# Optimization experiments

Measured on AMD Instinct MI355X. Metric: run time of the kernel, lower is better.

Reference implementation:

```python
import jax, jax.numpy as jnp
import numpy as np

B, N, DM = 8, 1024, 512
H, D = 8, 64  # heads, dim_head; inner_dim = H*D = 512

def setup_inputs() -> dict:
    key = jax.random.key(0)
    k1, k2, k3, k4, k5 = jax.random.split(key, 5)
    s = 1.0 / np.sqrt(DM)
    return {
        "current": jax.random.normal(k1, (B, N, DM), dtype=jnp.float32),
        "hidden": jax.random.normal(k2, (B, N, DM), dtype=jnp.float32),
        "Wq": jax.random.normal(k3, (DM, H * D), dtype=jnp.float32) * s,
        "Wkv": jax.random.normal(k4, (DM, 2 * H * D), dtype=jnp.float32) * s,
        "Wo": jax.random.normal(k5, (H * D, H * D), dtype=jnp.float32) * s,
    }

def reference(current, hidden, Wq, Wkv, Wo):
    b, n, _ = current.shape
    # projections (no bias, matching use_bias=False)
    q = (current @ Wq).reshape(b, n, H, D).transpose(0, 2, 1, 3)   # [B,H,N,D]
    kv = (hidden @ Wkv).reshape(b, n, 2, H, D).transpose(2, 0, 3, 1, 4)  # [2,B,H,N,D]
    k, v = kv[0], kv[1]
    # NOTE: original code computes self.scale but never applies it -> no scaling here
    dots = jnp.einsum('bhqd,bhkd->bhqk', q, k)                      # [B,H,N,N]
    attn = jax.nn.softmax(dots, axis=-1)
    out = jnp.einsum('bhqk,bhkd->bhqd', attn, v)                    # [B,H,N,D]
    out = out.transpose(0, 2, 1, 3).reshape(b, n, H * D)            # [B,N,inner]
    return out @ Wo  # dropout=0.0 -> identity
```

## Files before the change

### kernel.cpp

```cpp
#include <hip/hip_runtime.h>

typedef unsigned short ushort_t;
typedef __attribute__((ext_vector_type(8))) short short8;
typedef __attribute__((ext_vector_type(8))) _Float16 half8;
typedef __attribute__((ext_vector_type(4))) float f32x4;
typedef __attribute__((ext_vector_type(16))) float f32x16;
typedef __attribute__((ext_vector_type(2))) unsigned uint2v;
typedef __attribute__((ext_vector_type(4))) unsigned uint4v;

#define LOG2E 1.44269504088896f

__device__ __forceinline__ void async16(const void* g, void* l) {
  __builtin_amdgcn_global_load_lds(
      (const __attribute__((address_space(1))) void*)g,
      (__attribute__((address_space(3))) void*)l, 16, 0, 0);
}

__device__ __forceinline__ ushort_t f2h(float f) {
  union { _Float16 h; ushort_t u; } c; c.h = (_Float16)f; return c.u;
}

__device__ __forceinline__ half8 u4h8(uint4v u) { union { uint4v a; half8 b; } c; c.a = u; return c.b; }

__device__ __forceinline__ f32x16 zero16() {
  f32x16 v;
  #pragma unroll
  for (int i = 0; i < 16; i++) v[i] = 0.f;
  return v;
}

__global__ __launch_bounds__(256) void prep_all(const float* __restrict__ cur,
                                                const float* __restrict__ hid,
                                                const float* __restrict__ Wq,
                                                const float* __restrict__ Wkv,
                                                const float* __restrict__ Wo,
                                                ushort_t* __restrict__ ch,
                                                ushort_t* __restrict__ hh,
                                                ushort_t* __restrict__ qT,
                                                ushort_t* __restrict__ kvT,
                                                ushort_t* __restrict__ oT) {
  __shared__ float tile[32][33];
  int bid = blockIdx.x;
  if (bid >= 1024) {
    int i = (bid - 1024) * 256 + threadIdx.x;
    const float* src;
    ushort_t* dst;
    int j;
    if (i < 524288) { src = cur; dst = ch; j = i; }
    else            { src = hid; dst = hh; j = i - 524288; }
    const f32x4* s = (const f32x4*)src;
    f32x4 a = s[j * 2], b = s[j * 2 + 1];
    short8 o;
    #pragma unroll
    for (int k = 0; k < 4; k++) {
      o[k] = (short)f2h(a[k]);
      o[k + 4] = (short)f2h(b[k]);
    }
    ((short8*)dst)[j] = o;
    return;
  }
  const float* src; ushort_t* dh; int Nn, bx, by;
  const int K = 512;
  if (bid < 256)      { src = Wq;  dh = qT;  Nn = 512;  bx = (bid & 15) * 32; by = (bid >> 4) * 32; }
  else if (bid < 768) { int b = bid - 256; src = Wkv; dh = kvT; Nn = 1024; bx = (b & 31) * 32; by = (b >> 5) * 32; }
  else                { int b = bid - 768; src = Wo;  dh = oT;  Nn = 512;  bx = (b & 15) * 32; by = (b >> 4) * 32; }
  int tx = threadIdx.x & 31, ty = threadIdx.x >> 5;
  #pragma unroll
  for (int i = 0; i < 32; i += 8)
    tile[ty + i][tx] = src[(size_t)(by + ty + i) * Nn + bx + tx];
  __syncthreads();
  #pragma unroll
  for (int i = 0; i < 32; i += 8) {
    float v = tile[tx][ty + i];
    size_t idx = (size_t)(bx + ty + i) * K + by + tx;
    dh[idx] = f2h(v);
  }
}

template<int EPI>
__device__ __forceinline__ void gemm_body(const ushort_t* __restrict__ A,
                                          const ushort_t* __restrict__ B,
                                          ushort_t* __restrict__ o_16,
                                          ushort_t* __restrict__ o_vt,
                                          float* __restrict__ outf,
                                          int K, int ldo, int m0, int n0,
                                          ushort_t* lds) {
  constexpr int MT = 2, TN = 4;
  ushort_t* Ash = lds;
  ushort_t* Bsh = lds + 4096;
  const int tid = threadIdx.x;
  const int wave = tid >> 6, lane = tid & 63;
  const int wm = (wave >> 1) * 32, wn = (wave & 1) * 64;
  const int lrow = lane & 15, lq = lane >> 4;

  f32x4 acc[MT][TN];
  const f32x4 z = {0.f, 0.f, 0.f, 0.f};
  #pragma unroll
  for (int i = 0; i < MT; i++)
    #pragma unroll
    for (int j = 0; j < TN; j++) acc[i][j] = z;

  auto stage = [&](int k0, int d) {
    const int aoff = d * 2048, boff = d * 4096;
    {
      int r = tid >> 2, kc = tid & 3;
      int kcs = kc ^ ((r >> 1) & 3);
      async16(&A[(size_t)(m0 + r) * K + k0 + kcs * 8], &Ash[aoff + tid * 8]);
    }
    #pragma unroll
    for (int i = 0; i < 2; i++) {
      int g = i * 256 + tid;
      int r = g >> 2, kc = g & 3;
      int kcs = kc ^ ((r >> 1) & 3);
      async16(&B[(size_t)(n0 + r) * K + k0 + kcs * 8], &Bsh[boff + g * 8]);
    }
  };

  stage(0, 0);
  int cur = 0;
  for (int k0 = 0; k0 < K; k0 += 32) {
    if (k0 + 32 < K) {
      stage(k0 + 32, cur ^ 1);
      asm volatile("s_waitcnt vmcnt(3)" ::: "memory");
    } else {
      asm volatile("s_waitcnt vmcnt(0)" ::: "memory");
    }
    __builtin_amdgcn_s_barrier();

    const int ab = cur * 2048, bb = cur * 4096;
    half8 af[MT], bf[TN];
    #pragma unroll
    for (int t = 0; t < MT; t++) {
      int row = wm + t * 16 + lrow;
      af[t] = *(const half8*)&Ash[ab + row * 32 + (lq ^ ((row >> 1) & 3)) * 8];
    }
    #pragma unroll
    for (int t = 0; t < TN; t++) {
      int row = wn + t * 16 + lrow;
      bf[t] = *(const half8*)&Bsh[bb + row * 32 + (lq ^ ((row >> 1) & 3)) * 8];
    }
    #pragma unroll
    for (int ti = 0; ti < MT; ti++)
      #pragma unroll
      for (int tj = 0; tj < TN; tj++)
        acc[ti][tj] = __builtin_amdgcn_mfma_f32_16x16x32_f16(af[ti], bf[tj], acc[ti][tj], 0, 0, 0);

    if (k0 + 32 < K) {
      asm volatile("s_waitcnt lgkmcnt(0)" ::: "memory");
      __builtin_amdgcn_s_barrier();
    }
    cur ^= 1;
  }

  #pragma unroll
  for (int ti = 0; ti < MT; ti++) {
    #pragma unroll
    for (int tj = 0; tj < TN; tj++) {
      int row0 = m0 + wm + ti * 16 + lq * 4;
      int col = n0 + wn + tj * 16 + lrow;
      #pragma unroll
      for (int r = 0; r < 4; r++) {
        int m = row0 + r;
        float fv = acc[ti][tj][r];
        if (EPI == 0) {
          size_t idx = (size_t)((m >> 10) * 8 + (col >> 6)) * 65536 + (m & 1023) * 64 + (col & 63);
          o_16[idx] = f2h(fv);
        } else if (EPI == 1) {
          if (col < 512) {
            size_t idx = (size_t)((m >> 10) * 8 + (col >> 6)) * 65536 + (m & 1023) * 64 + (col & 63);
            o_16[idx] = f2h(fv);
          } else {
            int cc = col - 512;
            o_vt[(size_t)(((m >> 10) * 8 + (cc >> 6)) * 64 + (cc & 63)) * 1024 + (m & 1023)] = f2h(fv);
          }
        } else {
          outf[(size_t)m * ldo + col] = fv;
        }
      }
    }
  }
}

__global__ __launch_bounds__(256) void gemm_qkv(const ushort_t* __restrict__ H,
                                                const ushort_t* __restrict__ WkvT,
                                                ushort_t* __restrict__ ko,
                                                ushort_t* __restrict__ vt,
                                                const ushort_t* __restrict__ C,
                                                const ushort_t* __restrict__ WqT,
                                                ushort_t* __restrict__ qo) {
  __shared__ __align__(16) ushort_t lds[12288];
  int bid = blockIdx.x;
  int w = (bid & 7) * 192 + (bid >> 3);
  if (w < 1024) {
    int n0 = (w & 7) * 128, m0 = (w >> 3) * 64;
    gemm_body<1>(H, WkvT, ko, vt, (float*)nullptr, 512, 0, m0, n0, lds);
  } else {
    int ww = w - 1024;
    int n0 = (ww & 3) * 128, m0 = (ww >> 2) * 64;
    gemm_body<0>(C, WqT, qo, (ushort_t*)nullptr, (float*)nullptr, 512, 0, m0, n0, lds);
  }
}

__global__ __launch_bounds__(256) void gemm_o(const ushort_t* __restrict__ A,
                                              const ushort_t* __restrict__ B,
                                              float* __restrict__ outf) {
  __shared__ __align__(16) ushort_t lds[12288];
  int bid = blockIdx.x;
  int w = (bid & 7) * 64 + (bid >> 3);
  int n0 = (w & 3) * 128, m0 = (w >> 2) * 64;
  gemm_body<2>(A, B, (ushort_t*)nullptr, (ushort_t*)nullptr, outf, 512, 512, m0, n0, lds);
}

__global__ __launch_bounds__(256, 2) void flash_attn(const ushort_t* __restrict__ qb,
                                                     const ushort_t* __restrict__ kb,
                                                     const ushort_t* __restrict__ vtb,
                                                     ushort_t* __restrict__ ob) {
  __shared__ __align__(16) ushort_t Ksh[2][64 * 64];
  __shared__ __align__(16) ushort_t VTs[2][64 * 64];

  const int tid = threadIdx.x;
  const int wave = tid >> 6, lane = tid & 63;
  const int bh = blockIdx.x & 63, qt = blockIdx.x >> 6;
  const int l31 = lane & 31, hi = lane >> 5;

  const ushort_t* Q = qb + (size_t)bh * 65536;
  const ushort_t* Kp = kb + (size_t)bh * 65536;
  const ushort_t* VT = vtb + (size_t)bh * 65536;

  const int qrow0 = qt * 128 + wave * 32;

  half8 qf[4];
  #pragma unroll
  for (int ds = 0; ds < 4; ds++)
    qf[ds] = *(const half8*)&Q[(size_t)(qrow0 + l31) * 64 + ds * 16 + hi * 8];

  f32x16 oacc[2];
  oacc[0] = zero16();
  oacc[1] = zero16();
  float m_i = -1e30f, l_i = 0.f;

  const int r7 = l31 & 7;
  int pc[4];
  #pragma unroll
  for (int i = 0; i < 4; i++) pc[i] = (((2 * i + hi) ^ r7) << 3);
  const int ro0 = l31 * 64, ro1 = ro0 + 2048;

  auto stage = [&](int kt, int d) {
    #pragma unroll
    for (int i = 0; i < 2; i++) {
      int g = i * 256 + tid, rw = g >> 3, ch = g & 7;
      int co = ((ch ^ (rw & 7)) << 3);
      int lofs = rw * 64 + (ch << 3);
      async16(&Kp[(size_t)(kt * 64 + rw) * 64 + co], &Ksh[d][lofs]);
      async16(&VT[(size_t)rw * 1024 + kt * 64 + co], &VTs[d][lofs]);
    }
  };

  stage(0, 0);

  for (int kt = 0; kt < 16; kt++) {
    const int cur = kt & 1;
    if (kt < 15) {
      stage(kt + 1, cur ^ 1);
      asm volatile("s_waitcnt vmcnt(4)" ::: "memory");
    } else {
      asm volatile("s_waitcnt vmcnt(0)" ::: "memory");
    }
    __builtin_amdgcn_s_barrier();

    f32x16 sacc0 = zero16(), sacc1 = zero16();
    __builtin_amdgcn_s_setprio(1);
    #pragma unroll
    for (int ds = 0; ds < 4; ds++) {
      half8 k0 = *(const half8*)&Ksh[cur][ro0 + pc[ds]];
      half8 k1 = *(const half8*)&Ksh[cur][ro1 + pc[ds]];
      sacc0 = __builtin_amdgcn_mfma_f32_32x32x16_f16(k0, qf[ds], sacc0, 0, 0, 0);
      sacc1 = __builtin_amdgcn_mfma_f32_32x32x16_f16(k1, qf[ds], sacc1, 0, 0, 0);
    }
    __builtin_amdgcn_s_setprio(0);

    float mx = -1e30f;
    #pragma unroll
    for (int r = 0; r < 16; r++) {
      mx = fmaxf(mx, sacc0[r]);
      mx = fmaxf(mx, sacc1[r]);
    }
    mx = fmaxf(mx, __shfl_xor(mx, 32));
    float mnew = fmaxf(m_i, mx);
    float mL = mnew * LOG2E;
    float alpha = exp2f(fmaf(m_i, LOG2E, -mL));
    float sum = 0.f;
    unsigned pw[16];
    #pragma unroll
    for (int j = 0; j < 8; j++) {
      float p0 = exp2f(fmaf(sacc0[2 * j], LOG2E, -mL));
      float p1 = exp2f(fmaf(sacc0[2 * j + 1], LOG2E, -mL));
      sum += p0 + p1;
      asm("v_cvt_pkrtz_f16_f32 %0, %1, %2" : "=v"(pw[j]) : "v"(p0), "v"(p1));
    }
    #pragma unroll
    for (int j = 0; j < 8; j++) {
      float p0 = exp2f(fmaf(sacc1[2 * j], LOG2E, -mL));
      float p1 = exp2f(fmaf(sacc1[2 * j + 1], LOG2E, -mL));
      sum += p0 + p1;
      asm("v_cvt_pkrtz_f16_f32 %0, %1, %2" : "=v"(pw[8 + j]) : "v"(p0), "v"(p1));
    }
    sum += __shfl_xor(sum, 32);
    l_i = fmaf(l_i, alpha, sum);
    m_i = mnew;
    #pragma unroll
    for (int r = 0; r < 16; r++) {
      oacc[0][r] *= alpha;
      oacc[1][r] *= alpha;
    }

    __builtin_amdgcn_s_setprio(1);
    #pragma unroll
    for (int ks = 0; ks < 4; ks++) {
      const int base = (ks >> 1) * 8 + (ks & 1) * 4;
      uint2v s0 = __builtin_amdgcn_permlane32_swap(pw[base + 0], pw[base + 2], false, false);
      uint2v s1 = __builtin_amdgcn_permlane32_swap(pw[base + 1], pw[base + 3], false, false);
      half8 pfrag = u4h8((uint4v){s0.x, s1.x, s0.y, s1.y});
      half8 vf0 = *(const half8*)&VTs[cur][ro0 + pc[ks]];
      half8 vf1 = *(const half8*)&VTs[cur][ro1 + pc[ks]];
      oacc[0] = __builtin_amdgcn_mfma_f32_32x32x16_f16(vf0, pfrag, oacc[0], 0, 0, 0);
      oacc[1] = __builtin_amdgcn_mfma_f32_32x32x16_f16(vf1, pfrag, oacc[1], 0, 0, 0);
    }
    __builtin_amdgcn_s_setprio(0);

    if (kt < 15) {
      asm volatile("s_waitcnt lgkmcnt(0)" ::: "memory");
      __builtin_amdgcn_s_barrier();
    }
  }

  const int b = bh >> 3, h = bh & 7;
  const int n = qrow0 + l31;
  float rinv = 1.f / l_i;
  #pragma unroll
  for (int dt = 0; dt < 2; dt++) {
    #pragma unroll
    for (int t = 0; t < 4; t++) {
      ushort_t hv[4];
      #pragma unroll
      for (int e = 0; e < 4; e++)
        hv[e] = f2h(oacc[dt][4 * t + e] * rinv);
      size_t idx = (size_t)(b * 1024 + n) * 512 + h * 64 + dt * 32 + t * 8 + hi * 4;
      *(uint2v*)&ob[idx] = (uint2v){(unsigned)hv[0] | ((unsigned)hv[1] << 16),
                                    (unsigned)hv[2] | ((unsigned)hv[3] << 16)};
    }
  }
}

extern "C" void kernel_launch(void* const* d_in, const int* in_sizes, int n_in,
                              void* d_out, int out_size, void* d_ws, size_t ws_size,
                              hipStream_t stream) {
  const float* cur = (const float*)d_in[0];
  const float* hid = (const float*)d_in[1];
  const float* Wq  = (const float*)d_in[2];
  const float* Wkv = (const float*)d_in[3];
  const float* Wo  = (const float*)d_in[4];

  ushort_t* ws = (ushort_t*)d_ws;
  ushort_t* C   = ws;
  ushort_t* H   = C + 4194304;
  ushort_t* ko  = H + 4194304;
  ushort_t* vt  = ko + 4194304;
  ushort_t* qo  = vt + 4194304;
  ushort_t* WqT = qo + 4194304;
  ushort_t* WkvT = WqT + 262144;
  ushort_t* WoT = WkvT + 524288;

  prep_all<<<5120, 256, 0, stream>>>(cur, hid, Wq, Wkv, Wo, C, H, WqT, WkvT, WoT);

  gemm_qkv<<<1536, 256, 0, stream>>>(H, WkvT, ko, vt, C, WqT, qo);

  flash_attn<<<512, 256, 0, stream>>>(qo, ko, vt, C);

  gemm_o<<<512, 256, 0, stream>>>(C, WoT, (float*)d_out);
}
```

Before: 170.0 us.

## Triple-buffer GEMM K-loop and enlarge QKV GEMM tiles to 128x128

Templates the GEMM body on its per-wave tile counts and moves the K-loop from double to triple buffering, so loads are issued two stages ahead with matching vmcnt waits. The QKV projection GEMM moves to 128x128 block tiles, halving its grid, while the output GEMM keeps 64x128 but gains the third buffer. The aim is to hide global-load latency better and raise operand reuse. The cost is more LDS per block, more accumulator registers in the QKV GEMM, which can lower occupancy, and fewer blocks to spread across CUs.

```diff
diff --git a/kernel.cpp b/kernel.cpp
--- a/kernel.cpp
+++ b/kernel.cpp
@@ -77,7 +77,7 @@
   }
 }
 
-template<int EPI>
+template<int EPI, int MT, int TN>
 __device__ __forceinline__ void gemm_body(const ushort_t* __restrict__ A,
                                           const ushort_t* __restrict__ B,
                                           ushort_t* __restrict__ o_16,
@@ -85,12 +85,16 @@
                                           float* __restrict__ outf,
                                           int K, int ldo, int m0, int n0,
                                           ushort_t* lds) {
-  constexpr int MT = 2, TN = 4;
+  constexpr int BM = MT * 32;
+  constexpr int BN = TN * 32;
+  constexpr int ASZ = BM * 32;
+  constexpr int BSZ = BN * 32;
+  constexpr int LPS = (MT + TN) / 2;
   ushort_t* Ash = lds;
-  ushort_t* Bsh = lds + 4096;
+  ushort_t* Bsh = lds + 3 * ASZ;
   const int tid = threadIdx.x;
   const int wave = tid >> 6, lane = tid & 63;
-  const int wm = (wave >> 1) * 32, wn = (wave & 1) * 64;
+  const int wm = (wave >> 1) * (MT * 16), wn = (wave & 1) * (TN * 16);
   const int lrow = lane & 15, lq = lane >> 4;
 
   f32x4 acc[MT][TN];
@@ -100,15 +104,18 @@
     #pragma unroll
     for (int j = 0; j < TN; j++) acc[i][j] = z;
 
-  auto stage = [&](int k0, int d) {
-    const int aoff = d * 2048, boff = d * 4096;
-    {
-      int r = tid >> 2, kc = tid & 3;
+  auto stage = [&](int t, int d) {
+    const int k0 = t * 32;
+    const int aoff = d * ASZ, boff = d * BSZ;
+    #pragma unroll
+    for (int i = 0; i < MT / 2; i++) {
+      int g = i * 256 + tid;
+      int r = g >> 2, kc = g & 3;
       int kcs = kc ^ ((r >> 1) & 3);
-      async16(&A[(size_t)(m0 + r) * K + k0 + kcs * 8], &Ash[aoff + tid * 8]);
-    }
-    #pragma unroll
-    for (int i = 0; i < 2; i++) {
+      async16(&A[(size_t)(m0 + r) * K + k0 + kcs * 8], &Ash[aoff + g * 8]);
+    }
+    #pragma unroll
+    for (int i = 0; i < TN / 2; i++) {
       int g = i * 256 + tid;
       int r = g >> 2, kc = g & 3;
       int kcs = kc ^ ((r >> 1) & 3);
@@ -116,28 +123,34 @@
     }
   };
 
+  const int nt = K >> 5;
   stage(0, 0);
-  int cur = 0;
-  for (int k0 = 0; k0 < K; k0 += 32) {
-    if (k0 + 32 < K) {
-      stage(k0 + 32, cur ^ 1);
-      asm volatile("s_waitcnt vmcnt(3)" ::: "memory");
+  stage(1, 1);
+  for (int t = 0; t < nt; t++) {
+    if (t + 2 < nt) stage(t + 2, (t + 2) % 3);
+    if (t + 2 < nt) {
+      if constexpr (LPS == 4) asm volatile("s_waitcnt vmcnt(8)" ::: "memory");
+      else                    asm volatile("s_waitcnt vmcnt(6)" ::: "memory");
+    } else if (t + 1 < nt) {
+      if constexpr (LPS == 4) asm volatile("s_waitcnt vmcnt(4)" ::: "memory");
+      else                    asm volatile("s_waitcnt vmcnt(3)" ::: "memory");
     } else {
       asm volatile("s_waitcnt vmcnt(0)" ::: "memory");
     }
     __builtin_amdgcn_s_barrier();
 
-    const int ab = cur * 2048, bb = cur * 4096;
+    const int d = t % 3;
+    const int ab = d * ASZ, bb = d * BSZ;
     half8 af[MT], bf[TN];
     #pragma unroll
-    for (int t = 0; t < MT; t++) {
-      int row = wm + t * 16 + lrow;
-      af[t] = *(const half8*)&Ash[ab + row * 32 + (lq ^ ((row >> 1) & 3)) * 8];
-    }
-    #pragma unroll
-    for (int t = 0; t < TN; t++) {
-      int row = wn + t * 16 + lrow;
-      bf[t] = *(const half8*)&Bsh[bb + row * 32 + (lq ^ ((row >> 1) & 3)) * 8];
+    for (int ti = 0; ti < MT; ti++) {
+      int row = wm + ti * 16 + lrow;
+      af[ti] = *(const half8*)&Ash[ab + row * 32 + (lq ^ ((row >> 1) & 3)) * 8];
+    }
+    #pragma unroll
+    for (int tj = 0; tj < TN; tj++) {
+      int row = wn + tj * 16 + lrow;
+      bf[tj] = *(const half8*)&Bsh[bb + row * 32 + (lq ^ ((row >> 1) & 3)) * 8];
     }
     #pragma unroll
     for (int ti = 0; ti < MT; ti++)
@@ -145,11 +158,10 @@
       for (int tj = 0; tj < TN; tj++)
         acc[ti][tj] = __builtin_amdgcn_mfma_f32_16x16x32_f16(af[ti], bf[tj], acc[ti][tj], 0, 0, 0);
 
-    if (k0 + 32 < K) {
+    if (t + 1 < nt) {
       asm volatile("s_waitcnt lgkmcnt(0)" ::: "memory");
       __builtin_amdgcn_s_barrier();
     }
-    cur ^= 1;
   }
 
   #pragma unroll
@@ -188,27 +200,27 @@
                                                 const ushort_t* __restrict__ C,
                                                 const ushort_t* __restrict__ WqT,
                                                 ushort_t* __restrict__ qo) {
-  __shared__ __align__(16) ushort_t lds[12288];
+  __shared__ __align__(16) ushort_t lds[24576];
   int bid = blockIdx.x;
-  int w = (bid & 7) * 192 + (bid >> 3);
-  if (w < 1024) {
-    int n0 = (w & 7) * 128, m0 = (w >> 3) * 64;
-    gemm_body<1>(H, WkvT, ko, vt, (float*)nullptr, 512, 0, m0, n0, lds);
+  int w = (bid & 7) * 96 + (bid >> 3);
+  if (w < 512) {
+    int n0 = (w & 7) * 128, m0 = (w >> 3) * 128;
+    gemm_body<1, 4, 4>(H, WkvT, ko, vt, (float*)nullptr, 512, 0, m0, n0, lds);
   } else {
-    int ww = w - 1024;
-    int n0 = (ww & 3) * 128, m0 = (ww >> 2) * 64;
-    gemm_body<0>(C, WqT, qo, (ushort_t*)nullptr, (float*)nullptr, 512, 0, m0, n0, lds);
+    int ww = w - 512;
+    int n0 = (ww & 3) * 128, m0 = (ww >> 2) * 128;
+    gemm_body<0, 4, 4>(C, WqT, qo, (ushort_t*)nullptr, (float*)nullptr, 512, 0, m0, n0, lds);
   }
 }
 
 __global__ __launch_bounds__(256) void gemm_o(const ushort_t* __restrict__ A,
                                               const ushort_t* __restrict__ B,
                                               float* __restrict__ outf) {
-  __shared__ __align__(16) ushort_t lds[12288];
+  __shared__ __align__(16) ushort_t lds[18432];
   int bid = blockIdx.x;
   int w = (bid & 7) * 64 + (bid >> 3);
   int n0 = (w & 3) * 128, m0 = (w >> 2) * 64;
-  gemm_body<2>(A, B, (ushort_t*)nullptr, (ushort_t*)nullptr, outf, 512, 512, m0, n0, lds);
+  gemm_body<2, 2, 4>(A, B, (ushort_t*)nullptr, (ushort_t*)nullptr, outf, 512, 512, m0, n0, lds);
 }
 
 __global__ __launch_bounds__(256, 2) void flash_attn(const ushort_t* __restrict__ qb,
@@ -373,7 +385,7 @@
 
   prep_all<<<5120, 256, 0, stream>>>(cur, hid, Wq, Wkv, Wo, C, H, WqT, WkvT, WoT);
 
-  gemm_qkv<<<1536, 256, 0, stream>>>(H, WkvT, ko, vt, C, WqT, qo);
+  gemm_qkv<<<768, 256, 0, stream>>>(H, WkvT, ko, vt, C, WqT, qo);
 
   flash_attn<<<512, 256, 0, stream>>>(qo, ko, vt, C);
 
```

Result: faster. 166.5 us (median of 2 runs) (-2.1%).
